# Optimization experiments

Hardware: AMD Instinct MI355X
Metric: run time of the kernel (lower is better)

The kernel has to match this reference:

```python
import jax, jax.numpy as jnp
import numpy as np

B, S, N, F, H, O = 4, 16, 1024, 64, 128, 64
L_LAYERS, N_HEADS, CHUNK = 3, 4, 128
EPS = 1e-5


def setup_inputs() -> dict:
    key = jax.random.key(0)
    ks = jax.random.split(key, 16)
    adj = (jax.random.uniform(ks[0], (B, S, N, N)) < 0.05).astype(jnp.float32)
    adj = adj * (1.0 - jnp.eye(N, dtype=jnp.float32))
    x = jax.random.normal(ks[1], (B, S, F), dtype=jnp.float32)
    mask = jnp.ones((B, S), dtype=jnp.float32)
    sd = lambda fan_in: 1.0 / np.sqrt(fan_in)
    inp = {
        "x": x, "adj": adj, "mask": mask,
        "feature_importance": jnp.ones((F,), jnp.float32),
        "W_in": jax.random.normal(ks[2], (F, H)) * sd(F),
        "b_in": jnp.zeros((H,), jnp.float32),
        "ln_g": jnp.ones((H,), jnp.float32),
        "ln_b": jnp.zeros((H,), jnp.float32),
        "gcn_W": jax.random.normal(ks[3], (L_LAYERS, H, H)) * sd(H),
        "gcn_b": jnp.zeros((L_LAYERS, H), jnp.float32),
        "bn_g": jnp.ones((L_LAYERS, H), jnp.float32),
        "bn_b": jnp.zeros((L_LAYERS, H), jnp.float32),
        "Wqkv": jax.random.normal(ks[4], (3 * H, H)) * sd(H),
        "bqkv": jnp.zeros((3 * H,), jnp.float32),
        "Wo": jax.random.normal(ks[5], (H, H)) * sd(H),
        "bo": jnp.zeros((H,), jnp.float32),
        "W_out": jax.random.normal(ks[6], (H, O)) * sd(H),
        "b_out": jnp.zeros((O,), jnp.float32),
    }
    return inp


def _chunked_mha(h, Wqkv, bqkv, Wo, bo):
    # h: [B,S,N,H]; attention within chunks of CHUNK nodes (torch MHA, eval mode)
    b, s, n, hdim = h.shape
    c, dh = n // CHUNK, hdim // N_HEADS
    xr = h.reshape(b, s, c, CHUNK, hdim)
    qkv = xr @ Wqkv.T + bqkv                      # [B,S,C,L,3H]
    q, k, v = jnp.split(qkv, 3, axis=-1)
    split = lambda t: t.reshape(b, s, c, CHUNK, N_HEADS, dh).swapaxes(-3, -2)  # [B,S,C,nh,L,dh]
    q, k, v = split(q) * (dh ** -0.5), split(k), split(v)
    attn = jax.nn.softmax(jnp.einsum('bscnld,bscnmd->bscnlm', q, k), axis=-1)
    o = jnp.einsum('bscnlm,bscnmd->bscnld', attn, v)
    o = o.swapaxes(-3, -2).reshape(b, s, c, CHUNK, hdim) @ Wo.T + bo
    return o.reshape(b, s, n, hdim)


def reference(x, adj, mask, feature_importance, W_in, b_in, ln_g, ln_b,
              gcn_W, gcn_b, bn_g, bn_b, Wqkv, bqkv, Wo, bo, W_out, b_out):
    b, s, f = x.shape
    n = adj.shape[-1]
    # feature scaling + input projection + layer norm (same vector for all nodes)
    xv = (x * feature_importance) @ W_in + b_in            # [B,S,H]
    mu = xv.mean(-1, keepdims=True)
    var = ((xv - mu) ** 2).mean(-1, keepdims=True)
    hv = (xv - mu) / jnp.sqrt(var + EPS) * ln_g + ln_b
    h = jnp.broadcast_to(hv[:, :, None, :], (b, s, n, hv.shape[-1]))  # [B,S,N,H]
    h_init = h
    # GCN normalization: D^{-1/2} (A + I) D^{-1/2}
    A_hat = adj + jnp.eye(n, dtype=adj.dtype)
    dinv = jax.lax.rsqrt(A_hat.sum(-1))                     # [B,S,N]
    A_norm = dinv[..., :, None] * A_hat * dinv[..., None, :]
    bn_scale = 1.0 / np.sqrt(1.0 + EPS)  # eval BN, running mean 0 / var 1
    for l in range(L_LAYERS):
        hw = h @ gcn_W[l]
        hc = jnp.einsum('bsnm,bsmh->bsnh', A_norm, hw) + gcn_b[l]
        hc = hc * bn_scale * bn_g[l] + bn_b[l]
        hc = _chunked_mha(hc, Wqkv, bqkv, Wo, bo)
        hc = jax.nn.relu(hc)  # dropout = identity in eval
        h = h + hc            # use_skip (num_layers > 1)
    h = h + h_init
    node_embeddings = h @ W_out + b_out                    # [B,S,N,O]
    graph_embeddings = node_embeddings.mean(axis=2)        # [B,S,O]
    graph_embeddings = graph_embeddings * mask[:, :, None]
    node_embeddings = node_embeddings * mask[:, :, None, None]
    return node_embeddings, graph_embeddings
```

## Files before the change

### kernel.cpp

```cpp
#include <hip/hip_runtime.h>

typedef __bf16 bf16_t;
typedef bf16_t bf16x8 __attribute__((ext_vector_type(8)));
typedef float f32x4 __attribute__((ext_vector_type(4)));

#define DEV static __device__ __forceinline__

constexpr float kBnScale = 0.999995000037499375f;

DEV unsigned short f2bf(float f) {
  unsigned u = __builtin_bit_cast(unsigned, f);
  u += 0x7fffu + ((u >> 16) & 1u);
  return (unsigned short)(u >> 16);
}
DEV float bf2f(unsigned short s) {
  return __builtin_bit_cast(float, ((unsigned)s) << 16);
}
DEV f32x4 mfma16(bf16x8 a, bf16x8 b, f32x4 c) {
  return __builtin_amdgcn_mfma_f32_16x16x32_bf16(a, b, c, 0, 0, 0);
}
DEV unsigned swz(unsigned byteoff, unsigned row) { return byteoff ^ ((row & 7u) << 4); }

__global__ __launch_bounds__(256) void k_pre(
    const float* __restrict__ adj, unsigned short* __restrict__ cols,
    int* __restrict__ cnt, float* __restrict__ dinv,
    const float* __restrict__ x, const float* __restrict__ fi,
    const float* __restrict__ Win, const float* __restrict__ bin,
    const float* __restrict__ lng, const float* __restrict__ lnb,
    const float* __restrict__ gW, const float* __restrict__ bng,
    float* __restrict__ hv, float* __restrict__ hw0s,
    const float* __restrict__ Wqkv, const float* __restrict__ Wo,
    const float* __restrict__ Wout,
    unsigned short* __restrict__ WqkvB, unsigned short* __restrict__ WoB,
    unsigned short* __restrict__ gWB, unsigned short* __restrict__ WoutB) {
  const int bid = blockIdx.x;
  if (bid < 16384) {
    const int c4 = (bid & 7) * 2048 + (bid >> 3);
    const int w = threadIdx.x >> 6, lane = threadIdx.x & 63;
    const long row = (long)c4 * 4 + w;
    const float* ap = adj + row * 1024;
    unsigned short* cp = cols + row * 128;
    int c = 0;
#pragma unroll
    for (int it = 0; it < 4; ++it) {
      const float4 v4 = *(const float4*)(ap + it * 256 + lane * 4);
      const float vv[4] = {v4.x, v4.y, v4.z, v4.w};
#pragma unroll
      for (int j = 0; j < 4; ++j) {
        const unsigned long long m = __ballot(vv[j] != 0.0f);
        const int pos = c + __popcll(m & ((1ull << lane) - 1ull));
        if (vv[j] != 0.0f && pos < 128) cp[pos] = (unsigned short)(it * 256 + lane * 4 + j);
        c += __popcll(m);
      }
    }
    if (lane == 0) {
      cnt[row] = c;
      dinv[row] = 1.0f / sqrtf((float)(c + 1));
    }
  } else if (bid < 16448) {
    __shared__ float sred[2], sred2[2], shv[128];
    const int bs = bid - 16384, t = threadIdx.x;
    float accv = 0.f, d = 0.f;
    if (t < 128) {
      accv = bin[t];
      for (int f = 0; f < 64; ++f) accv += x[bs * 64 + f] * fi[f] * Win[f * 128 + t];
      float ssum = accv;
      for (int m = 1; m < 64; m <<= 1) ssum += __shfl_xor(ssum, m);
      if ((t & 63) == 0) sred[t >> 6] = ssum;
    }
    __syncthreads();
    const float mu = (sred[0] + sred[1]) * (1.0f / 128.0f);
    if (t < 128) {
      d = accv - mu;
      float vs = d * d;
      for (int m = 1; m < 64; m <<= 1) vs += __shfl_xor(vs, m);
      if ((t & 63) == 0) sred2[t >> 6] = vs;
    }
    __syncthreads();
    const float var = (sred2[0] + sred2[1]) * (1.0f / 128.0f);
    if (t < 128) {
      const float h = d / sqrtf(var + 1e-5f) * lng[t] + lnb[t];
      hv[bs * 128 + t] = h;
      shv[t] = h;
    }
    __syncthreads();
    if (t < 128) {
      float a2 = 0.f;
      for (int k = 0; k < 128; ++k) a2 += shv[k] * gW[k * 128 + t];
      hw0s[bs * 128 + t] = a2 * kBnScale * bng[t];
    }
  } else {
    const int i = (bid - 16448) * 256 + threadIdx.x;
    if (i < 49152) {
      WqkvB[i] = f2bf(Wqkv[i]);
    } else if (i < 65536) {
      const int j = i - 49152;
      WoB[j] = f2bf(Wo[j]);
    } else if (i < 114688) {
      const int j = i - 65536, l = j >> 14, r = j & 16383, n = r >> 7, k = r & 127;
      gWB[j] = f2bf(gW[(l << 14) + k * 128 + n]);
    } else {
      const int j = i - 114688, n = j >> 7, k = j & 127;
      WoutB[j] = f2bf(Wout[k * 64 + n]);
    }
  }
}

__global__ __launch_bounds__(256) void k_scal2(const unsigned short* __restrict__ cols,
                                               const int* __restrict__ cnt, const float* __restrict__ dinv,
                                               const float* __restrict__ hw0s,
                                               const float* __restrict__ gb0, const float* __restrict__ bng0,
                                               const float* __restrict__ bnb0,
                                               unsigned* __restrict__ hc0) {
  int b = blockIdx.x;
  b = (b & 7) * 2048 + (b >> 3);
  const int w = threadIdx.x >> 6, lane = threadIdx.x & 63;
  const long row = (long)b * 4 + w;
  const int cn = cnt[row] < 128 ? cnt[row] : 128;
  const long bsbase = row & ~1023L;
  const int c0 = cols[row * 128 + lane];
  const int c1 = cols[row * 128 + 64 + lane];
  float s = 0.f;
  if (lane < cn) s += dinv[bsbase + c0];
  if (lane + 64 < cn) s += dinv[bsbase + c1];
  for (int m = 1; m < 64; m <<= 1) s += __shfl_xor(s, m);
  const float d = dinv[row];
  const float S = d * (d + s);
  const int bs = (int)(row >> 10);
  const float2 hw = ((const float2*)hw0s)[bs * 64 + lane];
  const float2 g2 = ((const float2*)gb0)[lane];
  const float2 bg = ((const float2*)bng0)[lane];
  const float2 bb = ((const float2*)bnb0)[lane];
  const float v0 = S * hw.x + (g2.x * kBnScale * bg.x + bb.x);
  const float v1 = S * hw.y + (g2.y * kBnScale * bg.y + bb.y);
  hc0[row * 64 + lane] = (unsigned)f2bf(v0) | ((unsigned)f2bf(v1) << 16);
}

__global__ __launch_bounds__(256, 2) void k_qkv(const unsigned short* __restrict__ hc,
                                                const unsigned short* __restrict__ WqkvB,
                                                const float* __restrict__ bqkv,
                                                unsigned short* __restrict__ qkvb) {
  __shared__ __align__(16) unsigned short Ab[128 * 128];
  __shared__ __align__(16) unsigned short Bb[128 * 128];
  const int t = threadIdx.x;
  const int cx = (blockIdx.x & 7) * 64 + (blockIdx.x >> 3);
  const long blockRow = (long)cx * 128;
  const int lane = t & 63, w = t >> 6, wr = w >> 1, wc = w & 1;
  const int g = lane >> 4, l15 = lane & 15;
  const f32x4 vzero = {0.f, 0.f, 0.f, 0.f};

#pragma unroll
  for (int i = 0; i < 8; ++i) {
    const int f = (t + i * 256) * 8;
    const unsigned row = f >> 7, k = f & 127;
    *(uint4*)(Ab + (swz(row * 256u + k * 2u, row) >> 1)) = *(const uint4*)(hc + blockRow * 128 + f);
  }

#pragma unroll 1
  for (int pan = 0; pan < 3; ++pan) {
#pragma unroll
    for (int i = 0; i < 8; ++i) {
      const int f = (t + i * 256) * 8;
      const unsigned n = f >> 7, k = f & 127;
      *(uint4*)(Bb + (swz(n * 256u + k * 2u, n) >> 1)) = *(const uint4*)(WqkvB + pan * 16384 + f);
    }
    __syncthreads();

    f32x4 acc[4][4];
#pragma unroll
    for (int a = 0; a < 4; ++a)
#pragma unroll
      for (int b = 0; b < 4; ++b) acc[a][b] = vzero;
#pragma unroll
    for (int kk = 0; kk < 4; ++kk) {
      const unsigned kb = kk * 64u + (unsigned)(g << 4);
      bf16x8 af[4], bfr[4];
#pragma unroll
      for (int mt = 0; mt < 4; ++mt) {
        const unsigned row = wr * 64 + mt * 16 + l15;
        af[mt] = *(const bf16x8*)(Ab + (swz(row * 256u + kb, row) >> 1));
      }
#pragma unroll
      for (int nt = 0; nt < 4; ++nt) {
        const unsigned col = wc * 64 + nt * 16 + l15;
        bfr[nt] = *(const bf16x8*)(Bb + (swz(col * 256u + kb, col) >> 1));
      }
#pragma unroll
      for (int mt = 0; mt < 4; ++mt)
#pragma unroll
        for (int nt = 0; nt < 4; ++nt) acc[mt][nt] = mfma16(af[mt], bfr[nt], acc[mt][nt]);
    }
#pragma unroll
    for (int mt = 0; mt < 4; ++mt)
#pragma unroll
      for (int nt = 0; nt < 4; ++nt)
#pragma unroll
        for (int r = 0; r < 4; ++r) {
          const long gRow = blockRow + wr * 64 + mt * 16 + g * 4 + r;
          const int gCol = wc * 64 + nt * 16 + l15;
          qkvb[(size_t)pan * 8388608 + gRow * 128 + gCol] = f2bf(acc[mt][nt][r] + bqkv[pan * 128 + gCol]);
        }
    __syncthreads();
  }
}

__global__ __launch_bounds__(256) void k_spmm(const uint4* __restrict__ hwp16,
                                              const unsigned short* __restrict__ cols,
                                              const int* __restrict__ cnt, const float* __restrict__ dinv,
                                              const float* __restrict__ gb, const float* __restrict__ bng,
                                              const float* __restrict__ bnb, uint4* __restrict__ hc16) {
  int b = blockIdx.x;
  b = (b & 7) * 2048 + (b >> 3);
  const int w = threadIdx.x >> 6, lane = threadIdx.x & 63;
  const int g = lane >> 4, l15 = lane & 15;
  const long row = (long)b * 4 + w;
  __shared__ unsigned short scol[4][128];
  scol[w][lane] = cols[row * 128 + lane];
  scol[w][lane + 64] = cols[row * 128 + 64 + lane];
  const int cn = cnt[row] < 128 ? cnt[row] : 128;
  const long bsbase = row & ~1023L;
  float acc[8];
#pragma unroll
  for (int e = 0; e < 8; ++e) acc[e] = 0.f;
  if (g == 0) {
    const uint4 u = hwp16[row * 16 + l15];
    const unsigned uu[4] = {u.x, u.y, u.z, u.w};
#pragma unroll
    for (int e2 = 0; e2 < 4; ++e2) {
      acc[e2 * 2] += bf2f((unsigned short)uu[e2]);
      acc[e2 * 2 + 1] += bf2f((unsigned short)(uu[e2] >> 16));
    }
  }
  const int cn4 = cn & ~3;
#pragma unroll 2
  for (int i = 0; i < cn4; i += 4) {
    const int j = scol[w][i + g];
    const uint4 u = hwp16[(bsbase + j) * 16 + l15];
    const unsigned uu[4] = {u.x, u.y, u.z, u.w};
#pragma unroll
    for (int e2 = 0; e2 < 4; ++e2) {
      acc[e2 * 2] += bf2f((unsigned short)uu[e2]);
      acc[e2 * 2 + 1] += bf2f((unsigned short)(uu[e2] >> 16));
    }
  }
  if (cn4 + g < cn) {
    const int j = scol[w][cn4 + g];
    const uint4 u = hwp16[(bsbase + j) * 16 + l15];
    const unsigned uu[4] = {u.x, u.y, u.z, u.w};
#pragma unroll
    for (int e2 = 0; e2 < 4; ++e2) {
      acc[e2 * 2] += bf2f((unsigned short)uu[e2]);
      acc[e2 * 2 + 1] += bf2f((unsigned short)(uu[e2] >> 16));
    }
  }
#pragma unroll
  for (int e = 0; e < 8; ++e) {
    acc[e] += __shfl_xor(acc[e], 16);
    acc[e] += __shfl_xor(acc[e], 32);
  }
  if (g == 0) {
    const float di = dinv[row];
    const float4 gv0 = ((const float4*)gb)[l15 * 2], gv1 = ((const float4*)gb)[l15 * 2 + 1];
    const float4 bg0 = ((const float4*)bng)[l15 * 2], bg1 = ((const float4*)bng)[l15 * 2 + 1];
    const float4 bb0 = ((const float4*)bnb)[l15 * 2], bb1 = ((const float4*)bnb)[l15 * 2 + 1];
    float o[8];
    o[0] = (di * acc[0] + gv0.x) * (kBnScale * bg0.x) + bb0.x;
    o[1] = (di * acc[1] + gv0.y) * (kBnScale * bg0.y) + bb0.y;
    o[2] = (di * acc[2] + gv0.z) * (kBnScale * bg0.z) + bb0.z;
    o[3] = (di * acc[3] + gv0.w) * (kBnScale * bg0.w) + bb0.w;
    o[4] = (di * acc[4] + gv1.x) * (kBnScale * bg1.x) + bb1.x;
    o[5] = (di * acc[5] + gv1.y) * (kBnScale * bg1.y) + bb1.y;
    o[6] = (di * acc[6] + gv1.z) * (kBnScale * bg1.z) + bb1.z;
    o[7] = (di * acc[7] + gv1.w) * (kBnScale * bg1.w) + bb1.w;
    uint4 r;
    r.x = (unsigned)f2bf(o[0]) | ((unsigned)f2bf(o[1]) << 16);
    r.y = (unsigned)f2bf(o[2]) | ((unsigned)f2bf(o[3]) << 16);
    r.z = (unsigned)f2bf(o[4]) | ((unsigned)f2bf(o[5]) << 16);
    r.w = (unsigned)f2bf(o[6]) | ((unsigned)f2bf(o[7]) << 16);
    hc16[row * 16 + l15] = r;
  }
}

template <int MODE>
__global__ __launch_bounds__(256, 2) void k_af(
    const unsigned short* __restrict__ qkvb,
    const unsigned short* __restrict__ WoB, const unsigned short* __restrict__ B2,
    const float* __restrict__ bo, const float* __restrict__ hv,
    const float* __restrict__ dinv, const float* __restrict__ bout,
    const float* __restrict__ mask,
    unsigned short* __restrict__ hbufb, unsigned short* __restrict__ hwp,
    float* __restrict__ ne, float* __restrict__ gpart) {
  __shared__ __align__(16) unsigned short sm[32768];
  unsigned short* Ab = sm;
  unsigned short* Bb = sm + 16384;
  const int t = threadIdx.x, lane = t & 63, hd = t >> 6;
  const int g = lane >> 4, l15 = lane & 15;
  const int c = (blockIdx.x & 7) * 64 + (blockIdx.x >> 3);
  const long cb = (long)c * 128;
  const int bs = (int)(cb >> 10);
  const f32x4 vzero = {0.f, 0.f, 0.f, 0.f};
  const unsigned short* qp = qkvb;
  const unsigned short* kp = qkvb + 8388608;
  const unsigned short* vp = qkvb + 16777216;

  {
    const int m = t >> 1, half = t & 1;
    const unsigned short* vrow = vp + (cb + m) * 128 + half * 64;
#pragma unroll
    for (int c8 = 0; c8 < 8; ++c8) {
      const uint4 u = *(const uint4*)(vrow + c8 * 8);
      const int col0 = half * 64 + c8 * 8;
      unsigned short* vb = Ab + (col0 >> 5) * 4096;
      const int dh0 = col0 & 31;
      const unsigned short e[8] = {(unsigned short)u.x, (unsigned short)(u.x >> 16),
                                   (unsigned short)u.y, (unsigned short)(u.y >> 16),
                                   (unsigned short)u.z, (unsigned short)(u.z >> 16),
                                   (unsigned short)u.w, (unsigned short)(u.w >> 16)};
#pragma unroll
      for (int j = 0; j < 8; ++j) {
        const unsigned dh = dh0 + j;
        vb[swz(dh * 256u + (unsigned)m * 2u, dh) >> 1] = e[j];
      }
    }
  }
  bf16x8 kf[8];
#pragma unroll
  for (int nt = 0; nt < 8; ++nt)
    kf[nt] = *(const bf16x8*)(kp + (cb + nt * 16 + l15) * 128 + hd * 32 + (g << 3));
  __syncthreads();

  const unsigned short* vbb = Ab + hd * 4096;
  unsigned short* pb = Bb + hd * 4096;
  const float SC = 0.17677669529663687f * 1.4426950408889634f;
  unsigned pk[4][2][2][2];

#pragma unroll 1
  for (int p = 0; p < 4; ++p) {
    bf16x8 qf[2];
#pragma unroll
    for (int mt = 0; mt < 2; ++mt)
      qf[mt] = *(const bf16x8*)(qp + (cb + p * 32 + mt * 16 + l15) * 128 + hd * 32 + (g << 3));
    f32x4 s[2][8];
#pragma unroll
    for (int mt = 0; mt < 2; ++mt)
#pragma unroll
      for (int nt = 0; nt < 8; ++nt) s[mt][nt] = vzero;
#pragma unroll
    for (int nt = 0; nt < 8; ++nt)
#pragma unroll
      for (int mt = 0; mt < 2; ++mt) s[mt][nt] = mfma16(qf[mt], kf[nt], s[mt][nt]);

    float rinv[2][4];
#pragma unroll
    for (int mt = 0; mt < 2; ++mt) {
#pragma unroll
      for (int r = 0; r < 4; ++r) {
        float mx = s[mt][0][r];
#pragma unroll
        for (int nt = 1; nt < 8; ++nt) mx = fmaxf(mx, s[mt][nt][r]);
#pragma unroll
        for (int msk = 1; msk < 16; msk <<= 1) mx = fmaxf(mx, __shfl_xor(mx, msk));
        const unsigned qpr = mt * 16 + g * 4 + r;
        float sum = 0.f;
#pragma unroll
        for (int nt = 0; nt < 8; ++nt) {
          const float e = exp2f((s[mt][nt][r] - mx) * SC);
          sum += e;
          pb[swz(qpr * 256u + (nt * 16 + l15) * 2u, qpr) >> 1] = f2bf(e);
        }
#pragma unroll
        for (int msk = 1; msk < 16; msk <<= 1) sum += __shfl_xor(sum, msk);
        rinv[mt][r] = 1.0f / sum;
      }
    }

    f32x4 o[2][2];
#pragma unroll
    for (int mt = 0; mt < 2; ++mt)
#pragma unroll
      for (int nt = 0; nt < 2; ++nt) o[mt][nt] = vzero;
#pragma unroll
    for (int kk = 0; kk < 4; ++kk) {
      const unsigned kb = kk * 64u + (unsigned)(g << 4);
      bf16x8 pa[2], vf[2];
#pragma unroll
      for (int mt = 0; mt < 2; ++mt) {
        const unsigned rq = mt * 16 + l15;
        pa[mt] = *(const bf16x8*)(pb + (swz(rq * 256u + kb, rq) >> 1));
      }
#pragma unroll
      for (int nt = 0; nt < 2; ++nt) {
        const unsigned dh = nt * 16 + l15;
        vf[nt] = *(const bf16x8*)(vbb + (swz(dh * 256u + kb, dh) >> 1));
      }
#pragma unroll
      for (int mt = 0; mt < 2; ++mt)
#pragma unroll
        for (int nt = 0; nt < 2; ++nt) o[mt][nt] = mfma16(pa[mt], vf[nt], o[mt][nt]);
    }
#pragma unroll
    for (int mt = 0; mt < 2; ++mt)
#pragma unroll
      for (int nt = 0; nt < 2; ++nt) {
        pk[p][mt][nt][0] = (unsigned)f2bf(o[mt][nt][0] * rinv[mt][0]) |
                           ((unsigned)f2bf(o[mt][nt][1] * rinv[mt][1]) << 16);
        pk[p][mt][nt][1] = (unsigned)f2bf(o[mt][nt][2] * rinv[mt][2]) |
                           ((unsigned)f2bf(o[mt][nt][3] * rinv[mt][3]) << 16);
      }
  }
  __syncthreads();

#pragma unroll
  for (int p = 0; p < 4; ++p)
#pragma unroll
    for (int mt = 0; mt < 2; ++mt)
#pragma unroll
      for (int nt = 0; nt < 2; ++nt)
#pragma unroll
        for (int rr = 0; rr < 2; ++rr) {
          const unsigned u = pk[p][mt][nt][rr];
          const unsigned row0 = p * 32 + mt * 16 + g * 4 + rr * 2;
          const unsigned col = hd * 32 + nt * 16 + l15;
          Ab[swz(row0 * 256u + col * 2u, row0) >> 1] = (unsigned short)u;
          Ab[swz((row0 + 1) * 256u + col * 2u, row0 + 1) >> 1] = (unsigned short)(u >> 16);
        }
#pragma unroll
  for (int i = 0; i < 8; ++i) {
    const int f = (t + i * 256) * 8;
    const unsigned n = f >> 7, k = f & 127;
    *(uint4*)(Bb + (swz(n * 256u + k * 2u, n) >> 1)) = *(const uint4*)(WoB + f);
  }
  __syncthreads();

  const int wr = hd >> 1, wc = hd & 1;
  f32x4 acc[4][4];
#pragma unroll
  for (int a = 0; a < 4; ++a)
#pragma unroll
    for (int b = 0; b < 4; ++b) acc[a][b] = vzero;
#pragma unroll
  for (int kk = 0; kk < 4; ++kk) {
    const unsigned kb = kk * 64u + (unsigned)(g << 4);
    bf16x8 af[4], bfr[4];
#pragma unroll
    for (int mt = 0; mt < 4; ++mt) {
      const unsigned row = wr * 64 + mt * 16 + l15;
      af[mt] = *(const bf16x8*)(Ab + (swz(row * 256u + kb, row) >> 1));
    }
#pragma unroll
    for (int nt = 0; nt < 4; ++nt) {
      const unsigned col = wc * 64 + nt * 16 + l15;
      bfr[nt] = *(const bf16x8*)(Bb + (swz(col * 256u + kb, col) >> 1));
    }
#pragma unroll
    for (int mt = 0; mt < 4; ++mt)
#pragma unroll
      for (int nt = 0; nt < 4; ++nt) acc[mt][nt] = mfma16(af[mt], bfr[nt], acc[mt][nt]);
  }
  __syncthreads();

  {
    const float b0 = bo[wc * 64 + l15], b1 = bo[wc * 64 + 16 + l15];
    const float b2c = bo[wc * 64 + 32 + l15], b3c = bo[wc * 64 + 48 + l15];
    const float bb[4] = {b0, b1, b2c, b3c};
    float hb[4];
#pragma unroll
    for (int nt = 0; nt < 4; ++nt) hb[nt] = hv[bs * 128 + wc * 64 + nt * 16 + l15];
#pragma unroll
    for (int mt = 0; mt < 4; ++mt)
#pragma unroll
      for (int nt = 0; nt < 4; ++nt)
#pragma unroll
        for (int r = 0; r < 4; ++r) {
          const unsigned row = wr * 64 + mt * 16 + g * 4 + r;
          const long gRow = cb + row;
          const unsigned col = wc * 64 + nt * 16 + l15;
          float v = acc[mt][nt][r] + bb[nt];
          v = v > 0.f ? v : 0.f;
          if constexpr (MODE == 0) {
            v += hb[nt];
          } else {
            v += bf2f(hbufb[gRow * 128 + col]);
            if constexpr (MODE == 2) v += hb[nt];
          }
          const unsigned short vb = f2bf(v);
          if constexpr (MODE < 2) hbufb[gRow * 128 + col] = vb;
          Ab[swz(row * 256u + col * 2u, row) >> 1] = vb;
        }
  }
  if constexpr (MODE < 2) {
#pragma unroll
    for (int i = 0; i < 8; ++i) {
      const int f = (t + i * 256) * 8;
      const unsigned n = f >> 7, k = f & 127;
      *(uint4*)(Bb + (swz(n * 256u + k * 2u, n) >> 1)) = *(const uint4*)(B2 + f);
    }
  } else {
#pragma unroll
    for (int i = 0; i < 4; ++i) {
      const int f = (t + i * 256) * 8;
      const unsigned n = f >> 7, k = f & 127;
      *(uint4*)(Bb + (swz(n * 256u + k * 2u, n) >> 1)) = *(const uint4*)(B2 + f);
    }
  }
  __syncthreads();

  if constexpr (MODE < 2) {
#pragma unroll
    for (int a = 0; a < 4; ++a)
#pragma unroll
      for (int b = 0; b < 4; ++b) acc[a][b] = vzero;
#pragma unroll
    for (int kk = 0; kk < 4; ++kk) {
      const unsigned kb = kk * 64u + (unsigned)(g << 4);
      bf16x8 af[4], bfr[4];
#pragma unroll
      for (int mt = 0; mt < 4; ++mt) {
        const unsigned row = wr * 64 + mt * 16 + l15;
        af[mt] = *(const bf16x8*)(Ab + (swz(row * 256u + kb, row) >> 1));
      }
#pragma unroll
      for (int nt = 0; nt < 4; ++nt) {
        const unsigned col = wc * 64 + nt * 16 + l15;
        bfr[nt] = *(const bf16x8*)(Bb + (swz(col * 256u + kb, col) >> 1));
      }
#pragma unroll
      for (int mt = 0; mt < 4; ++mt)
#pragma unroll
        for (int nt = 0; nt < 4; ++nt) acc[mt][nt] = mfma16(af[mt], bfr[nt], acc[mt][nt]);
    }
#pragma unroll
    for (int mt = 0; mt < 4; ++mt)
#pragma unroll
      for (int nt = 0; nt < 4; ++nt)
#pragma unroll
        for (int r = 0; r < 4; ++r) {
          const long gRow = cb + wr * 64 + mt * 16 + g * 4 + r;
          const unsigned col = wc * 64 + nt * 16 + l15;
          hwp[gRow * 128 + col] = f2bf(acc[mt][nt][r] * dinv[gRow]);
        }
  } else {
    f32x4 acc2[4][2];
#pragma unroll
    for (int a = 0; a < 4; ++a)
#pragma unroll
      for (int b = 0; b < 2; ++b) acc2[a][b] = vzero;
#pragma unroll
    for (int kk = 0; kk < 4; ++kk) {
      const unsigned kb = kk * 64u + (unsigned)(g << 4);
      bf16x8 af[4], bfr[2];
#pragma unroll
      for (int mt = 0; mt < 4; ++mt) {
        const unsigned row = wr * 64 + mt * 16 + l15;
        af[mt] = *(const bf16x8*)(Ab + (swz(row * 256u + kb, row) >> 1));
      }
#pragma unroll
      for (int nt = 0; nt < 2; ++nt) {
        const unsigned col = wc * 32 + nt * 16 + l15;
        bfr[nt] = *(const bf16x8*)(Bb + (swz(col * 256u + kb, col) >> 1));
      }
#pragma unroll
      for (int mt = 0; mt < 4; ++mt)
#pragma unroll
        for (int nt = 0; nt < 2; ++nt) acc2[mt][nt] = mfma16(af[mt], bfr[nt], acc2[mt][nt]);
    }
    const float mk = mask[bs];
#pragma unroll
    for (int nt = 0; nt < 2; ++nt) {
      const unsigned col = wc * 32 + nt * 16 + l15;
      const float b2 = bout[col];
      float csum = 0.f;
#pragma unroll
      for (int mt = 0; mt < 4; ++mt)
#pragma unroll
        for (int r = 0; r < 4; ++r) {
          const long gRow = cb + wr * 64 + mt * 16 + g * 4 + r;
          const float v = (acc2[mt][nt][r] + b2) * mk;
          ne[gRow * 64 + col] = v;
          csum += v;
        }
      csum += __shfl_xor(csum, 16);
      csum += __shfl_xor(csum, 32);
      if (g == 0) gpart[((long)c * 2 + wr) * 64 + col] = csum;
    }
  }
}

__global__ void k_gfin(const float* __restrict__ gpart, float* __restrict__ ge) {
  const int tid = blockIdx.x * 256 + threadIdx.x;
  if (tid >= 4096) return;
  const int bs = tid >> 6, col = tid & 63;
  float s = 0.f;
#pragma unroll
  for (int q = 0; q < 16; ++q) s += gpart[(bs * 16 + q) * 64 + col];
  ge[tid] = s * (1.0f / 1024.0f);
}

extern "C" void kernel_launch(void* const* d_in, const int* in_sizes, int n_in,
                              void* d_out, int out_size, void* d_ws, size_t ws_size,
                              hipStream_t stream) {
  const float* x = (const float*)d_in[0];
  const float* adj = (const float*)d_in[1];
  const float* mask = (const float*)d_in[2];
  const float* fi = (const float*)d_in[3];
  const float* Win = (const float*)d_in[4];
  const float* bin = (const float*)d_in[5];
  const float* lng = (const float*)d_in[6];
  const float* lnb = (const float*)d_in[7];
  const float* gW = (const float*)d_in[8];
  const float* gB = (const float*)d_in[9];
  const float* bng = (const float*)d_in[10];
  const float* bnb = (const float*)d_in[11];
  const float* Wqkv = (const float*)d_in[12];
  const float* bqkv = (const float*)d_in[13];
  const float* Wo = (const float*)d_in[14];
  const float* bo = (const float*)d_in[15];
  const float* Wout = (const float*)d_in[16];
  const float* bout = (const float*)d_in[17];

  char* ws = (char*)d_ws;
  float* dinv = (float*)ws;                    ws += 65536 * 4;
  int* cnt = (int*)ws;                         ws += 65536 * 4;
  float* hv = (float*)ws;                      ws += 64 * 128 * 4;
  float* hw0s = (float*)ws;                    ws += 64 * 128 * 4;
  float* gpart = (float*)ws;                   ws += 1024 * 64 * 4;
  unsigned short* WqkvB = (unsigned short*)ws; ws += 49152 * 2;
  unsigned short* WoB = (unsigned short*)ws;   ws += 16384 * 2;
  unsigned short* gWB = (unsigned short*)ws;   ws += 49152 * 2;
  unsigned short* WoutB = (unsigned short*)ws; ws += 8192 * 2;
  unsigned short* cols = (unsigned short*)ws;  ws += (size_t)65536 * 128 * 2;
  unsigned short* hbufb = (unsigned short*)ws; ws += (size_t)65536 * 128 * 2;
  unsigned short* hwp = (unsigned short*)ws;   ws += (size_t)65536 * 128 * 2;
  unsigned short* hc = (unsigned short*)ws;    ws += (size_t)65536 * 128 * 2;
  unsigned short* qkvb = (unsigned short*)ws;  ws += (size_t)65536 * 384 * 2;

  float* ne = (float*)d_out;
  float* ge = ne + (size_t)4194304;

  k_pre<<<16928, 256, 0, stream>>>(adj, cols, cnt, dinv, x, fi, Win, bin, lng, lnb,
                                   gW, bng, hv, hw0s, Wqkv, Wo, Wout,
                                   WqkvB, WoB, gWB, WoutB);
  k_scal2<<<16384, 256, 0, stream>>>(cols, cnt, dinv, hw0s, gB, bng, bnb, (unsigned*)hc);

  k_qkv<<<512, 256, 0, stream>>>(hc, WqkvB, bqkv, qkvb);
  k_af<0><<<512, 256, 0, stream>>>(qkvb, WoB, gWB + 16384, bo, hv, dinv, nullptr, nullptr,
                                   hbufb, hwp, nullptr, nullptr);
  k_spmm<<<16384, 256, 0, stream>>>((const uint4*)hwp, cols, cnt, dinv,
                                    gB + 128, bng + 128, bnb + 128, (uint4*)hc);
  k_qkv<<<512, 256, 0, stream>>>(hc, WqkvB, bqkv, qkvb);
  k_af<1><<<512, 256, 0, stream>>>(qkvb, WoB, gWB + 32768, bo, hv, dinv, nullptr, nullptr,
                                   hbufb, hwp, nullptr, nullptr);
  k_spmm<<<16384, 256, 0, stream>>>((const uint4*)hwp, cols, cnt, dinv,
                                    gB + 256, bng + 256, bnb + 256, (uint4*)hc);
  k_qkv<<<512, 256, 0, stream>>>(hc, WqkvB, bqkv, qkvb);
  k_af<2><<<512, 256, 0, stream>>>(qkvb, WoB, WoutB, bo, hv, dinv, bout, mask,
                                   hbufb, nullptr, ne, gpart);

  k_gfin<<<16, 256, 0, stream>>>(gpart, ge);
}
```

Measured before the change: 348.7 us.

## Read weight fragments from global memory and shrink LDS to fit three blocks per CU

The weight matrices (Wqkv, Wo, B2) are no longer staged into shared memory. Their MFMA B fragments are loaded directly from global memory, where they should mostly hit in cache. The attention probability buffer is halved by handling one 16-row query tile at a time instead of two, and launch bounds are raised to three blocks per CU. The goal is higher occupancy and fewer LDS staging passes and barriers, at the cost of more global and L2 traffic for the weights and less instruction-level parallelism in the attention loop.

```diff
diff --git a/kernel.cpp b/kernel.cpp
--- a/kernel.cpp
+++ b/kernel.cpp
@@ -136,12 +136,11 @@
   hc0[row * 64 + lane] = (unsigned)f2bf(v0) | ((unsigned)f2bf(v1) << 16);
 }
 
-__global__ __launch_bounds__(256, 2) void k_qkv(const unsigned short* __restrict__ hc,
+__global__ __launch_bounds__(256, 3) void k_qkv(const unsigned short* __restrict__ hc,
                                                 const unsigned short* __restrict__ WqkvB,
                                                 const float* __restrict__ bqkv,
                                                 unsigned short* __restrict__ qkvb) {
   __shared__ __align__(16) unsigned short Ab[128 * 128];
-  __shared__ __align__(16) unsigned short Bb[128 * 128];
   const int t = threadIdx.x;
   const int cx = (blockIdx.x & 7) * 64 + (blockIdx.x >> 3);
   const long blockRow = (long)cx * 128;
@@ -155,17 +154,10 @@
     const unsigned row = f >> 7, k = f & 127;
     *(uint4*)(Ab + (swz(row * 256u + k * 2u, row) >> 1)) = *(const uint4*)(hc + blockRow * 128 + f);
   }
+  __syncthreads();
 
 #pragma unroll 1
   for (int pan = 0; pan < 3; ++pan) {
-#pragma unroll
-    for (int i = 0; i < 8; ++i) {
-      const int f = (t + i * 256) * 8;
-      const unsigned n = f >> 7, k = f & 127;
-      *(uint4*)(Bb + (swz(n * 256u + k * 2u, n) >> 1)) = *(const uint4*)(WqkvB + pan * 16384 + f);
-    }
-    __syncthreads();
-
     f32x4 acc[4][4];
 #pragma unroll
     for (int a = 0; a < 4; ++a)
@@ -174,6 +166,7 @@
 #pragma unroll
     for (int kk = 0; kk < 4; ++kk) {
       const unsigned kb = kk * 64u + (unsigned)(g << 4);
+      const unsigned ke = kk * 32u + (unsigned)(g << 3);
       bf16x8 af[4], bfr[4];
 #pragma unroll
       for (int mt = 0; mt < 4; ++mt) {
@@ -183,7 +176,7 @@
 #pragma unroll
       for (int nt = 0; nt < 4; ++nt) {
         const unsigned col = wc * 64 + nt * 16 + l15;
-        bfr[nt] = *(const bf16x8*)(Bb + (swz(col * 256u + kb, col) >> 1));
+        bfr[nt] = *(const bf16x8*)(WqkvB + (size_t)pan * 16384 + col * 128 + ke);
       }
 #pragma unroll
       for (int mt = 0; mt < 4; ++mt)
@@ -200,7 +193,6 @@
           const int gCol = wc * 64 + nt * 16 + l15;
           qkvb[(size_t)pan * 8388608 + gRow * 128 + gCol] = f2bf(acc[mt][nt][r] + bqkv[pan * 128 + gCol]);
         }
-    __syncthreads();
   }
 }
 
@@ -282,7 +274,7 @@
 }
 
 template <int MODE>
-__global__ __launch_bounds__(256, 2) void k_af(
+__global__ __launch_bounds__(256, 3) void k_af(
     const unsigned short* __restrict__ qkvb,
     const unsigned short* __restrict__ WoB, const unsigned short* __restrict__ B2,
     const float* __restrict__ bo, const float* __restrict__ hv,
@@ -290,9 +282,9 @@
     const float* __restrict__ mask,
     unsigned short* __restrict__ hbufb, unsigned short* __restrict__ hwp,
     float* __restrict__ ne, float* __restrict__ gpart) {
-  __shared__ __align__(16) unsigned short sm[32768];
-  unsigned short* Ab = sm;
-  unsigned short* Bb = sm + 16384;
+  __shared__ __align__(16) unsigned short sm[24576];
+  unsigned short* VT = sm;
+  unsigned short* Pr = sm + 16384;
   const int t = threadIdx.x, lane = t & 63, hd = t >> 6;
   const int g = lane >> 4, l15 = lane & 15;
   const int c = (blockIdx.x & 7) * 64 + (blockIdx.x >> 3);
@@ -310,7 +302,7 @@
     for (int c8 = 0; c8 < 8; ++c8) {
       const uint4 u = *(const uint4*)(vrow + c8 * 8);
       const int col0 = half * 64 + c8 * 8;
-      unsigned short* vb = Ab + (col0 >> 5) * 4096;
+      unsigned short* vb = VT + (col0 >> 5) * 4096;
       const int dh0 = col0 & 31;
       const unsigned short e[8] = {(unsigned short)u.x, (unsigned short)(u.x >> 16),
                                    (unsigned short)u.y, (unsigned short)(u.y >> 16),
@@ -329,84 +321,56 @@
     kf[nt] = *(const bf16x8*)(kp + (cb + nt * 16 + l15) * 128 + hd * 32 + (g << 3));
   __syncthreads();
 
-  const unsigned short* vbb = Ab + hd * 4096;
-  unsigned short* pb = Bb + hd * 4096;
+  const unsigned short* vbb = VT + hd * 4096;
+  unsigned short* pb = Pr + hd * 2048;
   const float SC = 0.17677669529663687f * 1.4426950408889634f;
   unsigned pk[4][2][2][2];
 
 #pragma unroll 1
   for (int p = 0; p < 4; ++p) {
-    bf16x8 qf[2];
-#pragma unroll
-    for (int mt = 0; mt < 2; ++mt)
-      qf[mt] = *(const bf16x8*)(qp + (cb + p * 32 + mt * 16 + l15) * 128 + hd * 32 + (g << 3));
-    f32x4 s[2][8];
-#pragma unroll
-    for (int mt = 0; mt < 2; ++mt)
-#pragma unroll
-      for (int nt = 0; nt < 8; ++nt) s[mt][nt] = vzero;
-#pragma unroll
-    for (int nt = 0; nt < 8; ++nt)
-#pragma unroll
-      for (int mt = 0; mt < 2; ++mt) s[mt][nt] = mfma16(qf[mt], kf[nt], s[mt][nt]);
-
-    float rinv[2][4];
-#pragma unroll
+#pragma unroll 1
     for (int mt = 0; mt < 2; ++mt) {
+      const bf16x8 qf = *(const bf16x8*)(qp + (cb + p * 32 + mt * 16 + l15) * 128 + hd * 32 + (g << 3));
+      f32x4 s[8];
+#pragma unroll
+      for (int nt = 0; nt < 8; ++nt) s[nt] = mfma16(qf, kf[nt], vzero);
+
+      float rinv[4];
 #pragma unroll
       for (int r = 0; r < 4; ++r) {
-        float mx = s[mt][0][r];
-#pragma unroll
-        for (int nt = 1; nt < 8; ++nt) mx = fmaxf(mx, s[mt][nt][r]);
+        float mx = s[0][r];
+#pragma unroll
+        for (int nt = 1; nt < 8; ++nt) mx = fmaxf(mx, s[nt][r]);
 #pragma unroll
         for (int msk = 1; msk < 16; msk <<= 1) mx = fmaxf(mx, __shfl_xor(mx, msk));
-        const unsigned qpr = mt * 16 + g * 4 + r;
+        const unsigned qpr = g * 4 + r;
         float sum = 0.f;
 #pragma unroll
         for (int nt = 0; nt < 8; ++nt) {
-          const float e = exp2f((s[mt][nt][r] - mx) * SC);
+          const float e = exp2f((s[nt][r] - mx) * SC);
           sum += e;
           pb[swz(qpr * 256u + (nt * 16 + l15) * 2u, qpr) >> 1] = f2bf(e);
         }
 #pragma unroll
         for (int msk = 1; msk < 16; msk <<= 1) sum += __shfl_xor(sum, msk);
-        rinv[mt][r] = 1.0f / sum;
-      }
-    }
-
-    f32x4 o[2][2];
-#pragma unroll
-    for (int mt = 0; mt < 2; ++mt)
-#pragma unroll
-      for (int nt = 0; nt < 2; ++nt) o[mt][nt] = vzero;
-#pragma unroll
-    for (int kk = 0; kk < 4; ++kk) {
-      const unsigned kb = kk * 64u + (unsigned)(g << 4);
-      bf16x8 pa[2], vf[2];
-#pragma unroll
-      for (int mt = 0; mt < 2; ++mt) {
-        const unsigned rq = mt * 16 + l15;
-        pa[mt] = *(const bf16x8*)(pb + (swz(rq * 256u + kb, rq) >> 1));
-      }
-#pragma unroll
-      for (int nt = 0; nt < 2; ++nt) {
-        const unsigned dh = nt * 16 + l15;
-        vf[nt] = *(const bf16x8*)(vbb + (swz(dh * 256u + kb, dh) >> 1));
-      }
-#pragma unroll
-      for (int mt = 0; mt < 2; ++mt)
-#pragma unroll
-        for (int nt = 0; nt < 2; ++nt) o[mt][nt] = mfma16(pa[mt], vf[nt], o[mt][nt]);
-    }
-#pragma unroll
-    for (int mt = 0; mt < 2; ++mt)
-#pragma unroll
-      for (int nt = 0; nt < 2; ++nt) {
-        pk[p][mt][nt][0] = (unsigned)f2bf(o[mt][nt][0] * rinv[mt][0]) |
-                           ((unsigned)f2bf(o[mt][nt][1] * rinv[mt][1]) << 16);
-        pk[p][mt][nt][1] = (unsigned)f2bf(o[mt][nt][2] * rinv[mt][2]) |
-                           ((unsigned)f2bf(o[mt][nt][3] * rinv[mt][3]) << 16);
-      }
+        rinv[r] = 1.0f / sum;
+      }
+
+      f32x4 o0 = vzero, o1 = vzero;
+#pragma unroll
+      for (int kk = 0; kk < 4; ++kk) {
+        const unsigned kb = kk * 64u + (unsigned)(g << 4);
+        const bf16x8 pa = *(const bf16x8*)(pb + (swz(l15 * 256u + kb, l15) >> 1));
+        const bf16x8 v0 = *(const bf16x8*)(vbb + (swz(l15 * 256u + kb, l15) >> 1));
+        const bf16x8 v1 = *(const bf16x8*)(vbb + (swz((16u + l15) * 256u + kb, 16 + l15) >> 1));
+        o0 = mfma16(pa, v0, o0);
+        o1 = mfma16(pa, v1, o1);
+      }
+      pk[p][mt][0][0] = (unsigned)f2bf(o0[0] * rinv[0]) | ((unsigned)f2bf(o0[1] * rinv[1]) << 16);
+      pk[p][mt][0][1] = (unsigned)f2bf(o0[2] * rinv[2]) | ((unsigned)f2bf(o0[3] * rinv[3]) << 16);
+      pk[p][mt][1][0] = (unsigned)f2bf(o1[0] * rinv[0]) | ((unsigned)f2bf(o1[1] * rinv[1]) << 16);
+      pk[p][mt][1][1] = (unsigned)f2bf(o1[2] * rinv[2]) | ((unsigned)f2bf(o1[3] * rinv[3]) << 16);
+    }
   }
   __syncthreads();
 
@@ -421,15 +385,9 @@
           const unsigned u = pk[p][mt][nt][rr];
           const unsigned row0 = p * 32 + mt * 16 + g * 4 + rr * 2;
           const unsigned col = hd * 32 + nt * 16 + l15;
-          Ab[swz(row0 * 256u + col * 2u, row0) >> 1] = (unsigned short)u;
-          Ab[swz((row0 + 1) * 256u + col * 2u, row0 + 1) >> 1] = (unsigned short)(u >> 16);
+          VT[swz(row0 * 256u + col * 2u, row0) >> 1] = (unsigned short)u;
+          VT[swz((row0 + 1) * 256u + col * 2u, row0 + 1) >> 1] = (unsigned short)(u >> 16);
         }
-#pragma unroll
-  for (int i = 0; i < 8; ++i) {
-    const int f = (t + i * 256) * 8;
-    const unsigned n = f >> 7, k = f & 127;
-    *(uint4*)(Bb + (swz(n * 256u + k * 2u, n) >> 1)) = *(const uint4*)(WoB + f);
-  }
   __syncthreads();
 
   const int wr = hd >> 1, wc = hd & 1;
@@ -441,16 +399,17 @@
 #pragma unroll
   for (int kk = 0; kk < 4; ++kk) {
     const unsigned kb = kk * 64u + (unsigned)(g << 4);
+    const unsigned ke = kk * 32u + (unsigned)(g << 3);
     bf16x8 af[4], bfr[4];
 #pragma unroll
     for (int mt = 0; mt < 4; ++mt) {
       const unsigned row = wr * 64 + mt * 16 + l15;
-      af[mt] = *(const bf16x8*)(Ab + (swz(row * 256u + kb, row) >> 1));
+      af[mt] = *(const bf16x8*)(VT + (swz(row * 256u + kb, row) >> 1));
     }
 #pragma unroll
     for (int nt = 0; nt < 4; ++nt) {
       const unsigned col = wc * 64 + nt * 16 + l15;
-      bfr[nt] = *(const bf16x8*)(Bb + (swz(col * 256u + kb, col) >> 1));
+      bfr[nt] = *(const bf16x8*)(WoB + col * 128 + ke);
     }
 #pragma unroll
     for (int mt = 0; mt < 4; ++mt)
@@ -485,23 +444,8 @@
           }
           const unsigned short vb = f2bf(v);
           if constexpr (MODE < 2) hbufb[gRow * 128 + col] = vb;
-          Ab[swz(row * 256u + col * 2u, row) >> 1] = vb;
+          VT[swz(row * 256u + col * 2u, row) >> 1] = vb;
         }
-  }
-  if constexpr (MODE < 2) {
-#pragma unroll
-    for (int i = 0; i < 8; ++i) {
-      const int f = (t + i * 256) * 8;
-      const unsigned n = f >> 7, k = f & 127;
-      *(uint4*)(Bb + (swz(n * 256u + k * 2u, n) >> 1)) = *(const uint4*)(B2 + f);
-    }
-  } else {
-#pragma unroll
-    for (int i = 0; i < 4; ++i) {
-      const int f = (t + i * 256) * 8;
-      const unsigned n = f >> 7, k = f & 127;
-      *(uint4*)(Bb + (swz(n * 256u + k * 2u, n) >> 1)) = *(const uint4*)(B2 + f);
-    }
   }
   __syncthreads();
 
@@ -513,16 +457,17 @@
 #pragma unroll
     for (int kk = 0; kk < 4; ++kk) {
       const unsigned kb = kk * 64u + (unsigned)(g << 4);
+      const unsigned ke = kk * 32u + (unsigned)(g << 3);
       bf16x8 af[4], bfr[4];
 #pragma unroll
       for (int mt = 0; mt < 4; ++mt) {
         const unsigned row = wr * 64 + mt * 16 + l15;
-        af[mt] = *(const bf16x8*)(Ab + (swz(row * 256u + kb, row) >> 1));
+        af[mt] = *(const bf16x8*)(VT + (swz(row * 256u + kb, row) >> 1));
       }
 #pragma unroll
       for (int nt = 0; nt < 4; ++nt) {
         const unsigned col = wc * 64 + nt * 16 + l15;
-        bfr[nt] = *(const bf16x8*)(Bb + (swz(col * 256u + kb, col) >> 1));
+        bfr[nt] = *(const bf16x8*)(B2 + col * 128 + ke);
       }
 #pragma unroll
       for (int mt = 0; mt < 4; ++mt)
@@ -548,16 +493,17 @@
 #pragma unroll
     for (int kk = 0; kk < 4; ++kk) {
       const unsigned kb = kk * 64u + (unsigned)(g << 4);
+      const unsigned ke = kk * 32u + (unsigned)(g << 3);
       bf16x8 af[4], bfr[2];
 #pragma unroll
       for (int mt = 0; mt < 4; ++mt) {
         const unsigned row = wr * 64 + mt * 16 + l15;
-        af[mt] = *(const bf16x8*)(Ab + (swz(row * 256u + kb, row) >> 1));
+        af[mt] = *(const bf16x8*)(VT + (swz(row * 256u + kb, row) >> 1));
       }
 #pragma unroll
       for (int nt = 0; nt < 2; ++nt) {
         const unsigned col = wc * 32 + nt * 16 + l15;
-        bfr[nt] = *(const bf16x8*)(Bb + (swz(col * 256u + kb, col) >> 1));
+        bfr[nt] = *(const bf16x8*)(B2 + col * 128 + ke);
       }
 #pragma unroll
       for (int mt = 0; mt < 4; ++mt)
```

Measured after the change: 395.8 us. +13.5%, slower.
